# Kernel tuning notes

Measured on AMD Instinct MI355X. Metric: run time of the kernel, lower is better.

The kernel has to match this reference:

```python
import jax, jax.numpy as jnp
import numpy as np

D_MODEL = 1024
NUM_HEADS = 16


def setup_inputs() -> dict:
    key = jax.random.key(0)
    ks = jax.random.split(key, 5)
    B, S, D = 2, 2048, D_MODEL
    scale = 1.0 / np.sqrt(D)
    return {
        "x": jax.random.normal(ks[0], (B, S, D), dtype=jnp.float32),
        "q_proj_weight": jax.random.normal(ks[1], (D, D), dtype=jnp.float32) * scale,
        "k_proj_weight": jax.random.normal(ks[2], (D, D), dtype=jnp.float32) * scale,
        "v_proj_weight": jax.random.normal(ks[3], (D, D), dtype=jnp.float32) * scale,
        "o_proj_weight": jax.random.normal(ks[4], (D, D), dtype=jnp.float32) * scale,
    }


def _attn(x, qw, kw, vw, ow, num_heads):
    B, S, D = x.shape
    d_k = D // num_heads
    q = x @ qw.T  # [B,S,D]
    k = x @ kw.T
    v = x @ vw.T
    # split heads: [B, H, S, d_k]
    q = q.reshape(B, S, num_heads, d_k).transpose(0, 2, 1, 3)
    k = k.reshape(B, S, num_heads, d_k).transpose(0, 2, 1, 3)
    v = v.reshape(B, S, num_heads, d_k).transpose(0, 2, 1, 3)
    scores = jnp.einsum('bhqd,bhkd->bhqk', q, k) / jnp.sqrt(jnp.asarray(d_k, x.dtype))
    causal = jnp.tril(jnp.ones((S, S), dtype=bool))  # [S,S]
    scores = jnp.where(causal[None, None], scores, jnp.asarray(-jnp.inf, x.dtype))
    attn = jax.nn.softmax(scores, axis=-1)
    out = jnp.einsum('bhqk,bhkd->bhqd', attn, v)  # [B,H,S,d_k]
    out = out.transpose(0, 2, 1, 3).reshape(B, S, D)
    return out @ ow.T


def reference(x, q_proj_weight, k_proj_weight, v_proj_weight, o_proj_weight):
    return _attn(x, q_proj_weight, k_proj_weight, v_proj_weight, o_proj_weight, NUM_HEADS)
```

## Files before the change

### kernel.cpp

```cpp
#include <hip/hip_runtime.h>

typedef __attribute__((ext_vector_type(8))) short short8;
typedef __attribute__((ext_vector_type(4))) float f32x4;

#define MFMA(a,b,c) __builtin_amdgcn_mfma_f32_16x16x32_bf16((a),(b),(c),0,0,0)

#define B_  2
#define S_  2048
#define D_  1024
#define H_  16
#define DK  64
#define KDIM 1024

typedef unsigned int u32;
typedef __attribute__((address_space(1))) const u32 gu32;
typedef __attribute__((address_space(3))) u32 lu32;

__device__ __forceinline__ void gll16(const unsigned short* g, unsigned short* l){
  __builtin_amdgcn_global_load_lds((gu32*)g, (lu32*)l, 16, 0, 0);
}

__device__ __forceinline__ unsigned short f2bf(float f){
  unsigned int u = __float_as_uint(f);
  u += 0x7fffu + ((u >> 16) & 1u);
  return (unsigned short)(u >> 16);
}

__device__ __forceinline__ u32 pkbf(float lo, float hi){
  u32 a = __float_as_uint(lo) + 0x8000u;
  u32 b = __float_as_uint(hi) + 0x8000u;
  return __builtin_amdgcn_perm(b, a, 0x07060302u);
}

__global__ void cvt_all(const float* __restrict__ x,  const float* __restrict__ qw,
                        const float* __restrict__ kw, const float* __restrict__ vw,
                        const float* __restrict__ ow,
                        unsigned short* __restrict__ xb,  unsigned short* __restrict__ wqb,
                        unsigned short* __restrict__ wkb, unsigned short* __restrict__ wvb,
                        unsigned short* __restrict__ wob,
                        int n4x, int n4w){
  int i = blockIdx.x * 256 + threadIdx.x;
  const float* src; unsigned short* dst; int n4;
  switch (blockIdx.y) {
    case 0:  src = x;  dst = xb;  n4 = n4x; break;
    case 1:  src = qw; dst = wqb; n4 = n4w; break;
    case 2:  src = kw; dst = wkb; n4 = n4w; break;
    case 3:  src = vw; dst = wvb; n4 = n4w; break;
    default: src = ow; dst = wob; n4 = n4w; break;
  }
  if (i >= n4) return;
  float4 f = reinterpret_cast<const float4*>(src)[i];
  ushort4 u;
  u.x = f2bf(f.x); u.y = f2bf(f.y); u.z = f2bf(f.z); u.w = f2bf(f.w);
  reinterpret_cast<ushort4*>(dst)[i] = u;
}

__global__ __launch_bounds__(256) void gemm_qkv(
    const unsigned short* __restrict__ X,
    const unsigned short* __restrict__ Wq,
    const unsigned short* __restrict__ Wk,
    const unsigned short* __restrict__ Wv,
    unsigned short* __restrict__ Qo,
    unsigned short* __restrict__ Ko,
    unsigned short* __restrict__ Vo)
{
  const int z = blockIdx.z;
  const unsigned short* __restrict__ W = (z == 0) ? Wq : (z == 1) ? Wk : Wv;
  const int n0 = blockIdx.x * 128;
  const int m0 = blockIdx.y * 128;

  __shared__ unsigned short As[128 * 64];
  __shared__ unsigned short Bs[128 * 64];

  const int tid  = threadIdx.x;
  const int wid  = tid >> 6, lane = tid & 63;
  const int wm   = (wid >> 1) * 64, wn = (wid & 1) * 64;
  const int lr   = lane & 15, c = lane >> 4;
  const int sw   = lr & 7;
  const int pc0  = (c ^ sw) * 8;
  const int pc1  = ((4 + c) ^ sw) * 8;

  const int srow = lane >> 3;
  const int scol = ((lane & 7) ^ srow) * 8;
  const unsigned short* gA = X + (size_t)(m0 + wid * 32 + srow) * KDIM + scol;
  const unsigned short* gB = W + (size_t)(n0 + wid * 32 + srow) * KDIM + scol;
  unsigned short* lA = &As[(wid * 32) * 64];
  unsigned short* lB = &Bs[(wid * 32) * 64];

  f32x4 acc[4][4];
  const f32x4 z4 = {0.f, 0.f, 0.f, 0.f};
  for (int i = 0; i < 4; i++)
    for (int j = 0; j < 4; j++) acc[i][j] = z4;

  for (int k0 = 0; k0 < KDIM; k0 += 64) {
    __syncthreads();
#pragma unroll
    for (int i = 0; i < 4; i++) gll16(gA + (size_t)(i * 8) * KDIM + k0, lA + i * 512);
#pragma unroll
    for (int i = 0; i < 4; i++) gll16(gB + (size_t)(i * 8) * KDIM + k0, lB + i * 512);
    __syncthreads();

    short8 a[4], b[4];
#pragma unroll
    for (int i = 0; i < 4; i++) a[i] = *(const short8*)&As[(wm + i * 16 + lr) * 64 + pc0];
#pragma unroll
    for (int j = 0; j < 4; j++) b[j] = *(const short8*)&Bs[(wn + j * 16 + lr) * 64 + pc0];
    if (z == 2) {
#pragma unroll
      for (int i = 0; i < 4; i++)
#pragma unroll
        for (int j = 0; j < 4; j++)
          acc[i][j] = MFMA(b[j], a[i], acc[i][j]);
    } else {
#pragma unroll
      for (int i = 0; i < 4; i++)
#pragma unroll
        for (int j = 0; j < 4; j++)
          acc[i][j] = MFMA(a[i], b[j], acc[i][j]);
    }
#pragma unroll
    for (int i = 0; i < 4; i++) a[i] = *(const short8*)&As[(wm + i * 16 + lr) * 64 + pc1];
#pragma unroll
    for (int j = 0; j < 4; j++) b[j] = *(const short8*)&Bs[(wn + j * 16 + lr) * 64 + pc1];
    if (z == 2) {
#pragma unroll
      for (int i = 0; i < 4; i++)
#pragma unroll
        for (int j = 0; j < 4; j++)
          acc[i][j] = MFMA(b[j], a[i], acc[i][j]);
    } else {
#pragma unroll
      for (int i = 0; i < 4; i++)
#pragma unroll
        for (int j = 0; j < 4; j++)
          acc[i][j] = MFMA(a[i], b[j], acc[i][j]);
    }
  }

  const int rbase = (lane >> 4) * 4;
  if (z == 2) {
    for (int i = 0; i < 4; i++)
      for (int j = 0; j < 4; j++)
        for (int r = 0; r < 4; r++) {
          int dfull = n0 + wn + j * 16 + rbase + r;
          int sfull = m0 + wm + i * 16 + lr;
          int h = dfull >> 6, d = dfull & 63;
          int bb = sfull >> 11, s = sfull & 2047;
          Vo[(((bb * H_ + h) * DK) + d) * S_ + s] = f2bf(acc[i][j][r]);
        }
  } else {
    for (int i = 0; i < 4; i++)
      for (int j = 0; j < 4; j++)
        for (int r = 0; r < 4; r++) {
          int m = m0 + wm + i * 16 + rbase + r;
          int n = n0 + wn + j * 16 + lr;
          float v = acc[i][j][r];
          int bb = m >> 11, s = m & 2047, h = n >> 6, d = n & 63;
          if (z == 0) {
            v *= 0.18033688f;
            Qo[(((bb * H_ + h) * S_) + s) * DK + d] = f2bf(v);
          } else {
            Ko[(((bb * H_ + h) * S_) + s) * DK + d] = f2bf(v);
          }
        }
  }
}

__global__ __launch_bounds__(512, 4) void attn(
    const unsigned short* __restrict__ Q,
    const unsigned short* __restrict__ K,
    const unsigned short* __restrict__ V,
    unsigned short* __restrict__ O)
{
  const int h = blockIdx.y, b = blockIdx.z;
  const int qt = b ? (15 - blockIdx.x) : blockIdx.x;

  const unsigned short* __restrict__ Qh = Q + (size_t)((b * H_ + h) * S_) * DK;
  const unsigned short* __restrict__ Kh = K + (size_t)((b * H_ + h) * S_) * DK;
  const unsigned short* __restrict__ Vh = V + (size_t)((b * H_ + h) * DK) * S_;

  __shared__ unsigned short Ks0[64 * 64];
  __shared__ unsigned short Ks1[64 * 64];
  __shared__ unsigned short Vs0[64 * 64];
  __shared__ unsigned short Vs1[64 * 64];
  __shared__ unsigned short Ps[8][16][72];

  const int tid = threadIdx.x, wid = tid >> 6, lane = tid & 63;
  const int lr = lane & 15;
  const int row4 = (lane >> 4) * 4;
  const int q0 = qt * 128;
  const int qcol = q0 + wid * 16 + lr;
  const int qwmin = q0 + wid * 16;
  const int qwmax = qwmin + 15;
  const int lk = (lane >> 4) * 8;

  const int pc0 = (((lane >> 4) + lr) & 7) * 8;
  const int pc1 = (((lane >> 4) + 4 + lr) & 7) * 8;

  const int sr8 = lane >> 3;
  const int sc8 = lane & 7;
  const int sg  = (sc8 - sr8) & 7;
  const int stRow = wid * 8 + sr8;
  const unsigned short* gK = Kh + (size_t)stRow * DK + sg * 8;
  const unsigned short* gV = Vh + (size_t)stRow * S_ + sg * 8;
  unsigned short* lK0 = &Ks0[wid * 8 * 64];
  unsigned short* lK1 = &Ks1[wid * 8 * 64];
  unsigned short* lV0 = &Vs0[wid * 8 * 64];
  unsigned short* lV1 = &Vs1[wid * 8 * 64];

  const short ONE = (short)0x3F80;
  const short8 ones = {ONE, ONE, ONE, ONE, ONE, ONE, ONE, ONE};

  short8 qf[2];
  qf[0] = *(const short8*)&Qh[(q0 + wid * 16 + lr) * DK + lk];
  qf[1] = *(const short8*)&Qh[(q0 + wid * 16 + lr) * DK + 32 + lk];

  const f32x4 z4 = {0.f, 0.f, 0.f, 0.f};
  f32x4 o[4];
  for (int i = 0; i < 4; i++) o[i] = z4;
  f32x4 rs = z4;

  auto tile = [&](int k0, const unsigned short* KS, const unsigned short* VS){
    if (k0 > qwmax) return;
    f32x4 sc[4];
    for (int nt = 0; nt < 4; nt++) {
      short8 kb0 = *(const short8*)&KS[(nt * 16 + lr) * 64 + pc0];
      short8 kb1 = *(const short8*)&KS[(nt * 16 + lr) * 64 + pc1];
      f32x4 s = MFMA(kb0, qf[0], z4);
      sc[nt] = MFMA(kb1, qf[1], s);
    }
    if (k0 + 63 > qwmin) {
      for (int nt = 0; nt < 4; nt++) {
        int kg = k0 + nt * 16 + row4;
        for (int r = 0; r < 4; r++)
          if (kg + r > qcol) sc[nt][r] = -INFINITY;
      }
    }
    for (int nt = 0; nt < 4; nt++) {
      float p0 = __builtin_amdgcn_exp2f(sc[nt][0]);
      float p1 = __builtin_amdgcn_exp2f(sc[nt][1]);
      float p2 = __builtin_amdgcn_exp2f(sc[nt][2]);
      float p3 = __builtin_amdgcn_exp2f(sc[nt][3]);
      uint2 pk;
      pk.x = pkbf(p0, p1);
      pk.y = pkbf(p2, p3);
      *(uint2*)&Ps[wid][lr][nt * 16 + row4] = pk;
    }
    short8 pf0 = *(const short8*)&Ps[wid][lr][lk];
    short8 pf1 = *(const short8*)&Ps[wid][lr][32 + lk];
    rs = MFMA(ones, pf0, rs);
    rs = MFMA(ones, pf1, rs);
    for (int dt = 0; dt < 4; dt++) {
      short8 vb0 = *(const short8*)&VS[(dt * 16 + lr) * 64 + pc0];
      short8 vb1 = *(const short8*)&VS[(dt * 16 + lr) * 64 + pc1];
      o[dt] = MFMA(vb0, pf0, o[dt]);
      o[dt] = MFMA(vb1, pf1, o[dt]);
    }
  };

  const int kt_end = 2 * qt + 2;

  gll16(gK, lK0);
  gll16(gV, lV0);

  for (int kt = 0; kt < kt_end; kt += 2) {
    const int k0 = kt * 64;
    __syncthreads();
    {
      gll16(gK + (size_t)(k0 + 64) * DK, lK1);
      gll16(gV + (k0 + 64),              lV1);
    }
    tile(k0, Ks0, Vs0);
    __syncthreads();
    if (kt + 2 < kt_end) {
      gll16(gK + (size_t)(k0 + 128) * DK, lK0);
      gll16(gV + (k0 + 128),              lV0);
    }
    tile(k0 + 64, Ks1, Vs1);
  }

  const float inv = 1.0f / rs[0];

  const int srow = q0 + wid * 16 + lr;
  for (int dt = 0; dt < 4; dt++) {
    uint2 pk;
    pk.x = pkbf(o[dt][0] * inv, o[dt][1] * inv);
    pk.y = pkbf(o[dt][2] * inv, o[dt][3] * inv);
    *(uint2*)&O[(size_t)(b * S_ + srow) * D_ + h * DK + dt * 16 + row4] = pk;
  }
}

__global__ __launch_bounds__(256) void gemm_oproj(
    const unsigned short* __restrict__ A,
    const unsigned short* __restrict__ W,
    float* __restrict__ out)
{
  const int n0 = blockIdx.x * 128;
  const int m0 = blockIdx.y * 128;

  __shared__ unsigned short As[128 * 64];
  __shared__ unsigned short Bs[128 * 64];

  const int tid  = threadIdx.x;
  const int wid  = tid >> 6, lane = tid & 63;
  const int wm   = (wid >> 1) * 64, wn = (wid & 1) * 64;
  const int lr   = lane & 15, c = lane >> 4;
  const int sw   = lr & 7;
  const int pc0  = (c ^ sw) * 8;
  const int pc1  = ((4 + c) ^ sw) * 8;

  const int srow = lane >> 3;
  const int scol = ((lane & 7) ^ srow) * 8;
  const unsigned short* gA = A + (size_t)(m0 + wid * 32 + srow) * KDIM + scol;
  const unsigned short* gB = W + (size_t)(n0 + wid * 32 + srow) * KDIM + scol;
  unsigned short* lA = &As[(wid * 32) * 64];
  unsigned short* lB = &Bs[(wid * 32) * 64];

  f32x4 acc[4][4];
  const f32x4 z4 = {0.f, 0.f, 0.f, 0.f};
  for (int i = 0; i < 4; i++)
    for (int j = 0; j < 4; j++) acc[i][j] = z4;

  for (int k0 = 0; k0 < KDIM; k0 += 64) {
    __syncthreads();
#pragma unroll
    for (int i = 0; i < 4; i++) gll16(gA + (size_t)(i * 8) * KDIM + k0, lA + i * 512);
#pragma unroll
    for (int i = 0; i < 4; i++) gll16(gB + (size_t)(i * 8) * KDIM + k0, lB + i * 512);
    __syncthreads();

    short8 a[4], b[4];
#pragma unroll
    for (int i = 0; i < 4; i++) a[i] = *(const short8*)&As[(wm + i * 16 + lr) * 64 + pc0];
#pragma unroll
    for (int j = 0; j < 4; j++) b[j] = *(const short8*)&Bs[(wn + j * 16 + lr) * 64 + pc0];
#pragma unroll
    for (int i = 0; i < 4; i++)
#pragma unroll
      for (int j = 0; j < 4; j++)
        acc[i][j] = MFMA(a[i], b[j], acc[i][j]);
#pragma unroll
    for (int i = 0; i < 4; i++) a[i] = *(const short8*)&As[(wm + i * 16 + lr) * 64 + pc1];
#pragma unroll
    for (int j = 0; j < 4; j++) b[j] = *(const short8*)&Bs[(wn + j * 16 + lr) * 64 + pc1];
#pragma unroll
    for (int i = 0; i < 4; i++)
#pragma unroll
      for (int j = 0; j < 4; j++)
        acc[i][j] = MFMA(a[i], b[j], acc[i][j]);
  }

  const int rbase = (lane >> 4) * 4;
  for (int i = 0; i < 4; i++)
    for (int j = 0; j < 4; j++)
      for (int r = 0; r < 4; r++) {
        int m = m0 + wm + i * 16 + rbase + r;
        int n = n0 + wn + j * 16 + lr;
        out[(size_t)m * D_ + n] = acc[i][j][r];
      }
}

extern "C" void kernel_launch(void* const* d_in, const int* in_sizes, int n_in,
                              void* d_out, int out_size, void* d_ws, size_t ws_size,
                              hipStream_t stream) {
  const float* x  = (const float*)d_in[0];
  const float* qw = (const float*)d_in[1];
  const float* kw = (const float*)d_in[2];
  const float* vw = (const float*)d_in[3];
  const float* ow = (const float*)d_in[4];
  float* out = (float*)d_out;

  char* ws = (char*)d_ws;
  size_t off = 0;
  auto alloc = [&](size_t bytes) -> void* {
    void* p = ws + off;
    off += (bytes + 255) & ~(size_t)255;
    return p;
  };
  const size_t XN = (size_t)B_ * S_ * D_;
  const size_t WN = (size_t)D_ * D_;
  unsigned short* xb  = (unsigned short*)alloc(XN * 2);
  unsigned short* wqb = (unsigned short*)alloc(WN * 2);
  unsigned short* wkb = (unsigned short*)alloc(WN * 2);
  unsigned short* wvb = (unsigned short*)alloc(WN * 2);
  unsigned short* wob = (unsigned short*)alloc(WN * 2);
  unsigned short* Qb  = (unsigned short*)alloc(XN * 2);
  unsigned short* Kb  = (unsigned short*)alloc(XN * 2);
  unsigned short* Vb  = (unsigned short*)alloc(XN * 2);
  unsigned short* Ob  = (unsigned short*)alloc(XN * 2);

  cvt_all<<<dim3((XN / 4 + 255) / 256, 5), dim3(256), 0, stream>>>(
      x, qw, kw, vw, ow, xb, wqb, wkb, wvb, wob, (int)(XN / 4), (int)(WN / 4));

  gemm_qkv<<<dim3(D_ / 128, (B_ * S_) / 128, 3), dim3(256), 0, stream>>>(
      xb, wqb, wkb, wvb, Qb, Kb, Vb);

  attn<<<dim3(S_ / 128, H_, B_), dim3(512), 0, stream>>>(Qb, Kb, Vb, Ob);

  gemm_oproj<<<dim3(D_ / 128, (B_ * S_) / 128), dim3(256), 0, stream>>>(Ob, wob, out);
}
```

Before: 177.2 us.

## Double-buffer LDS in projection GEMMs and shrink N tile to 64

Both the QKV and output-projection GEMMs now use two LDS buffers, prefetching the next two K-tiles with async global-to-LDS loads while MFMAs run on the current tile. Explicit vmcnt/lgkmcnt waits and barriers replace the two __syncthreads per iteration. The block N-tile drops from 128 to 64, doubling the grid for more parallelism across CUs. In exchange, per-block reuse of the A tile falls and the hand-placed waitcnt sequencing is fragile.

```diff
diff --git a/kernel.cpp b/kernel.cpp
--- a/kernel.cpp
+++ b/kernel.cpp
@@ -55,6 +55,8 @@
   reinterpret_cast<ushort4*>(dst)[i] = u;
 }
 
+struct Frags { short8 a0[4], a1[4], b0[2], b1[2]; };
+
 __global__ __launch_bounds__(256) void gemm_qkv(
     const unsigned short* __restrict__ X,
     const unsigned short* __restrict__ Wq,
@@ -66,81 +68,108 @@
 {
   const int z = blockIdx.z;
   const unsigned short* __restrict__ W = (z == 0) ? Wq : (z == 1) ? Wk : Wv;
-  const int n0 = blockIdx.x * 128;
+  const int n0 = blockIdx.x * 64;
   const int m0 = blockIdx.y * 128;
 
-  __shared__ unsigned short As[128 * 64];
-  __shared__ unsigned short Bs[128 * 64];
+  __shared__ unsigned short As[2][128 * 64];
+  __shared__ unsigned short Bs[2][64 * 64];
 
   const int tid  = threadIdx.x;
   const int wid  = tid >> 6, lane = tid & 63;
-  const int wm   = (wid >> 1) * 64, wn = (wid & 1) * 64;
+  const int wm   = (wid >> 1) * 64, wn = (wid & 1) * 32;
   const int lr   = lane & 15, c = lane >> 4;
   const int sw   = lr & 7;
   const int pc0  = (c ^ sw) * 8;
-  const int pc1  = ((4 + c) ^ sw) * 8;
+  const int pc1  = ((c ^ 4) ^ sw) * 8;
 
   const int srow = lane >> 3;
   const int scol = ((lane & 7) ^ srow) * 8;
   const unsigned short* gA = X + (size_t)(m0 + wid * 32 + srow) * KDIM + scol;
-  const unsigned short* gB = W + (size_t)(n0 + wid * 32 + srow) * KDIM + scol;
-  unsigned short* lA = &As[(wid * 32) * 64];
-  unsigned short* lB = &Bs[(wid * 32) * 64];
-
-  f32x4 acc[4][4];
+  const unsigned short* gB = W + (size_t)(n0 + wid * 16 + srow) * KDIM + scol;
+
+  auto stage = [&](int buf, int k0) {
+    unsigned short* la = &As[buf][(wid * 32) * 64];
+    unsigned short* lb = &Bs[buf][(wid * 16) * 64];
+#pragma unroll
+    for (int i = 0; i < 4; i++) gll16(gA + (size_t)(i * 8) * KDIM + k0, la + i * 512);
+#pragma unroll
+    for (int i = 0; i < 2; i++) gll16(gB + (size_t)(i * 8) * KDIM + k0, lb + i * 512);
+  };
+
+  auto ldfr = [&](int buf, Frags& f) {
+    const unsigned short* AS = As[buf];
+    const unsigned short* BS = Bs[buf];
+#pragma unroll
+    for (int i = 0; i < 4; i++) {
+      f.a0[i] = *(const short8*)&AS[(wm + i * 16 + lr) * 64 + pc0];
+      f.a1[i] = *(const short8*)&AS[(wm + i * 16 + lr) * 64 + pc1];
+    }
+#pragma unroll
+    for (int j = 0; j < 2; j++) {
+      f.b0[j] = *(const short8*)&BS[(wn + j * 16 + lr) * 64 + pc0];
+      f.b1[j] = *(const short8*)&BS[(wn + j * 16 + lr) * 64 + pc1];
+    }
+  };
+
+  f32x4 acc[4][2];
   const f32x4 z4 = {0.f, 0.f, 0.f, 0.f};
   for (int i = 0; i < 4; i++)
-    for (int j = 0; j < 4; j++) acc[i][j] = z4;
-
-  for (int k0 = 0; k0 < KDIM; k0 += 64) {
-    __syncthreads();
-#pragma unroll
-    for (int i = 0; i < 4; i++) gll16(gA + (size_t)(i * 8) * KDIM + k0, lA + i * 512);
-#pragma unroll
-    for (int i = 0; i < 4; i++) gll16(gB + (size_t)(i * 8) * KDIM + k0, lB + i * 512);
-    __syncthreads();
-
-    short8 a[4], b[4];
-#pragma unroll
-    for (int i = 0; i < 4; i++) a[i] = *(const short8*)&As[(wm + i * 16 + lr) * 64 + pc0];
-#pragma unroll
-    for (int j = 0; j < 4; j++) b[j] = *(const short8*)&Bs[(wn + j * 16 + lr) * 64 + pc0];
+    for (int j = 0; j < 2; j++) acc[i][j] = z4;
+
+  auto mfmas = [&](const Frags& f) {
     if (z == 2) {
 #pragma unroll
       for (int i = 0; i < 4; i++)
 #pragma unroll
-        for (int j = 0; j < 4; j++)
-          acc[i][j] = MFMA(b[j], a[i], acc[i][j]);
+        for (int j = 0; j < 2; j++) {
+          acc[i][j] = MFMA(f.b0[j], f.a0[i], acc[i][j]);
+          acc[i][j] = MFMA(f.b1[j], f.a1[i], acc[i][j]);
+        }
     } else {
 #pragma unroll
       for (int i = 0; i < 4; i++)
 #pragma unroll
-        for (int j = 0; j < 4; j++)
-          acc[i][j] = MFMA(a[i], b[j], acc[i][j]);
-    }
-#pragma unroll
-    for (int i = 0; i < 4; i++) a[i] = *(const short8*)&As[(wm + i * 16 + lr) * 64 + pc1];
-#pragma unroll
-    for (int j = 0; j < 4; j++) b[j] = *(const short8*)&Bs[(wn + j * 16 + lr) * 64 + pc1];
-    if (z == 2) {
-#pragma unroll
-      for (int i = 0; i < 4; i++)
-#pragma unroll
-        for (int j = 0; j < 4; j++)
-          acc[i][j] = MFMA(b[j], a[i], acc[i][j]);
-    } else {
-#pragma unroll
-      for (int i = 0; i < 4; i++)
-#pragma unroll
-        for (int j = 0; j < 4; j++)
-          acc[i][j] = MFMA(a[i], b[j], acc[i][j]);
-    }
-  }
+        for (int j = 0; j < 2; j++) {
+          acc[i][j] = MFMA(f.a0[i], f.b0[j], acc[i][j]);
+          acc[i][j] = MFMA(f.a1[i], f.b1[j], acc[i][j]);
+        }
+    }
+  };
+
+  stage(0, 0);
+  stage(1, 64);
+
+  Frags f;
+  const int NT = KDIM / 64;
+  for (int t = 0; t < NT - 2; ++t) {
+    const int buf = t & 1;
+    asm volatile("s_waitcnt vmcnt(6)" ::: "memory");
+    __builtin_amdgcn_s_barrier();
+    asm volatile("" ::: "memory");
+    ldfr(buf, f);
+    asm volatile("s_waitcnt lgkmcnt(0)" ::: "memory");
+    __builtin_amdgcn_sched_barrier(0);
+    __builtin_amdgcn_s_barrier();
+    asm volatile("" ::: "memory");
+    stage(buf, (t + 2) * 64);
+    __builtin_amdgcn_sched_barrier(0);
+    mfmas(f);
+  }
+  asm volatile("s_waitcnt vmcnt(6)" ::: "memory");
+  __builtin_amdgcn_s_barrier();
+  asm volatile("" ::: "memory");
+  ldfr((NT - 2) & 1, f);
+  mfmas(f);
+  asm volatile("s_waitcnt vmcnt(0)" ::: "memory");
+  __builtin_amdgcn_s_barrier();
+  asm volatile("" ::: "memory");
+  ldfr((NT - 1) & 1, f);
+  mfmas(f);
 
   const int rbase = (lane >> 4) * 4;
   if (z == 2) {
     for (int i = 0; i < 4; i++)
-      for (int j = 0; j < 4; j++)
+      for (int j = 0; j < 2; j++)
         for (int r = 0; r < 4; r++) {
           int dfull = n0 + wn + j * 16 + rbase + r;
           int sfull = m0 + wm + i * 16 + lr;
@@ -150,7 +179,7 @@
         }
   } else {
     for (int i = 0; i < 4; i++)
-      for (int j = 0; j < 4; j++)
+      for (int j = 0; j < 2; j++)
         for (int r = 0; r < 4; r++) {
           int m = m0 + wm + i * 16 + rbase + r;
           int n = n0 + wn + j * 16 + lr;
@@ -295,64 +324,97 @@
     const unsigned short* __restrict__ W,
     float* __restrict__ out)
 {
-  const int n0 = blockIdx.x * 128;
+  const int n0 = blockIdx.x * 64;
   const int m0 = blockIdx.y * 128;
 
-  __shared__ unsigned short As[128 * 64];
-  __shared__ unsigned short Bs[128 * 64];
+  __shared__ unsigned short As[2][128 * 64];
+  __shared__ unsigned short Bs[2][64 * 64];
 
   const int tid  = threadIdx.x;
   const int wid  = tid >> 6, lane = tid & 63;
-  const int wm   = (wid >> 1) * 64, wn = (wid & 1) * 64;
+  const int wm   = (wid >> 1) * 64, wn = (wid & 1) * 32;
   const int lr   = lane & 15, c = lane >> 4;
   const int sw   = lr & 7;
   const int pc0  = (c ^ sw) * 8;
-  const int pc1  = ((4 + c) ^ sw) * 8;
+  const int pc1  = ((c ^ 4) ^ sw) * 8;
 
   const int srow = lane >> 3;
   const int scol = ((lane & 7) ^ srow) * 8;
   const unsigned short* gA = A + (size_t)(m0 + wid * 32 + srow) * KDIM + scol;
-  const unsigned short* gB = W + (size_t)(n0 + wid * 32 + srow) * KDIM + scol;
-  unsigned short* lA = &As[(wid * 32) * 64];
-  unsigned short* lB = &Bs[(wid * 32) * 64];
-
-  f32x4 acc[4][4];
+  const unsigned short* gB = W + (size_t)(n0 + wid * 16 + srow) * KDIM + scol;
+
+  auto stage = [&](int buf, int k0) {
+    unsigned short* la = &As[buf][(wid * 32) * 64];
+    unsigned short* lb = &Bs[buf][(wid * 16) * 64];
+#pragma unroll
+    for (int i = 0; i < 4; i++) gll16(gA + (size_t)(i * 8) * KDIM + k0, la + i * 512);
+#pragma unroll
+    for (int i = 0; i < 2; i++) gll16(gB + (size_t)(i * 8) * KDIM + k0, lb + i * 512);
+  };
+
+  auto ldfr = [&](int buf, Frags& f) {
+    const unsigned short* AS = As[buf];
+    const unsigned short* BS = Bs[buf];
+#pragma unroll
+    for (int i = 0; i < 4; i++) {
+      f.a0[i] = *(const short8*)&AS[(wm + i * 16 + lr) * 64 + pc0];
+      f.a1[i] = *(const short8*)&AS[(wm + i * 16 + lr) * 64 + pc1];
+    }
+#pragma unroll
+    for (int j = 0; j < 2; j++) {
+      f.b0[j] = *(const short8*)&BS[(wn + j * 16 + lr) * 64 + pc0];
+      f.b1[j] = *(const short8*)&BS[(wn + j * 16 + lr) * 64 + pc1];
+    }
+  };
+
+  f32x4 acc[4][2];
   const f32x4 z4 = {0.f, 0.f, 0.f, 0.f};
   for (int i = 0; i < 4; i++)
-    for (int j = 0; j < 4; j++) acc[i][j] = z4;
-
-  for (int k0 = 0; k0 < KDIM; k0 += 64) {
-    __syncthreads();
-#pragma unroll
-    for (int i = 0; i < 4; i++) gll16(gA + (size_t)(i * 8) * KDIM + k0, lA + i * 512);
-#pragma unroll
-    for (int i = 0; i < 4; i++) gll16(gB + (size_t)(i * 8) * KDIM + k0, lB + i * 512);
-    __syncthreads();
-
-    short8 a[4], b[4];
-#pragma unroll
-    for (int i = 0; i < 4; i++) a[i] = *(const short8*)&As[(wm + i * 16 + lr) * 64 + pc0];
-#pragma unroll
-    for (int j = 0; j < 4; j++) b[j] = *(const short8*)&Bs[(wn + j * 16 + lr) * 64 + pc0];
+    for (int j = 0; j < 2; j++) acc[i][j] = z4;
+
+  auto mfmas = [&](const Frags& f) {
 #pragma unroll
     for (int i = 0; i < 4; i++)
 #pragma unroll
-      for (int j = 0; j < 4; j++)
-        acc[i][j] = MFMA(a[i], b[j], acc[i][j]);
-#pragma unroll
-    for (int i = 0; i < 4; i++) a[i] = *(const short8*)&As[(wm + i * 16 + lr) * 64 + pc1];
-#pragma unroll
-    for (int j = 0; j < 4; j++) b[j] = *(const short8*)&Bs[(wn + j * 16 + lr) * 64 + pc1];
-#pragma unroll
-    for (int i = 0; i < 4; i++)
-#pragma unroll
-      for (int j = 0; j < 4; j++)
-        acc[i][j] = MFMA(a[i], b[j], acc[i][j]);
-  }
+      for (int j = 0; j < 2; j++) {
+        acc[i][j] = MFMA(f.a0[i], f.b0[j], acc[i][j]);
+        acc[i][j] = MFMA(f.a1[i], f.b1[j], acc[i][j]);
+      }
+  };
+
+  stage(0, 0);
+  stage(1, 64);
+
+  Frags f;
+  const int NT = KDIM / 64;
+  for (int t = 0; t < NT - 2; ++t) {
+    const int buf = t & 1;
+    asm volatile("s_waitcnt vmcnt(6)" ::: "memory");
+    __builtin_amdgcn_s_barrier();
+    asm volatile("" ::: "memory");
+    ldfr(buf, f);
+    asm volatile("s_waitcnt lgkmcnt(0)" ::: "memory");
+    __builtin_amdgcn_sched_barrier(0);
+    __builtin_amdgcn_s_barrier();
+    asm volatile("" ::: "memory");
+    stage(buf, (t + 2) * 64);
+    __builtin_amdgcn_sched_barrier(0);
+    mfmas(f);
+  }
+  asm volatile("s_waitcnt vmcnt(6)" ::: "memory");
+  __builtin_amdgcn_s_barrier();
+  asm volatile("" ::: "memory");
+  ldfr((NT - 2) & 1, f);
+  mfmas(f);
+  asm volatile("s_waitcnt vmcnt(0)" ::: "memory");
+  __builtin_amdgcn_s_barrier();
+  asm volatile("" ::: "memory");
+  ldfr((NT - 1) & 1, f);
+  mfmas(f);
 
   const int rbase = (lane >> 4) * 4;
   for (int i = 0; i < 4; i++)
-    for (int j = 0; j < 4; j++)
+    for (int j = 0; j < 2; j++)
       for (int r = 0; r < 4; r++) {
         int m = m0 + wm + i * 16 + rbase + r;
         int n = n0 + wn + j * 16 + lr;
@@ -392,10 +454,10 @@
   cvt_all<<<dim3((XN / 4 + 255) / 256, 5), dim3(256), 0, stream>>>(
       x, qw, kw, vw, ow, xb, wqb, wkb, wvb, wob, (int)(XN / 4), (int)(WN / 4));
 
-  gemm_qkv<<<dim3(D_ / 128, (B_ * S_) / 128, 3), dim3(256), 0, stream>>>(
+  gemm_qkv<<<dim3(D_ / 64, (B_ * S_) / 128, 3), dim3(256), 0, stream>>>(
       xb, wqb, wkb, wvb, Qb, Kb, Vb);
 
   attn<<<dim3(S_ / 128, H_, B_), dim3(512), 0, stream>>>(Qb, Kb, Vb, Ob);
 
-  gemm_oproj<<<dim3(D_ / 128, (B_ * S_) / 128), dim3(256), 0, stream>>>(Ob, wob, out);
-}
+  gemm_oproj<<<dim3(D_ / 64, (B_ * S_) / 128), dim3(256), 0, stream>>>(Ob, wob, out);
+}
```

Result: faster. 162.8 us (-8.1%).
